# Performance work log

Hardware: AMD Instinct MI355X
Metric: run time of the kernel (lower is better)

The kernel has to match this reference:

```python
import jax, jax.numpy as jnp
import numpy as np
from jax import lax

KH = KW = 3
K = KH * KW
STRIDE = 1
PAD = 1
DIL = 1
GN_GROUPS = 32
EPS = 1e-5


def setup_inputs() -> dict:
    key = jax.random.key(0)
    k0, k1, k2 = jax.random.split(key, 3)
    B, C, H, W = 8, 256, 64, 64
    O = 256
    x = jax.random.normal(k0, (B, C, H, W), jnp.float32)
    # offset-predicting conv (DeformConv2dPack.conv_offset); small weights keep offsets ~O(1)
    w_off = jax.random.normal(k1, (2 * K, C, KH, KW), jnp.float32) * 0.01
    b_off = jnp.zeros((2 * K,), jnp.float32)
    w_dcn = jax.random.normal(k2, (O, C, KH, KW), jnp.float32) * (1.0 / np.sqrt(C * K))
    gamma = jnp.ones((O,), jnp.float32)
    beta = jnp.zeros((O,), jnp.float32)
    return {"x": x, "w_off": w_off, "b_off": b_off, "w_dcn": w_dcn, "gamma": gamma, "beta": beta}


def _deform_conv(x, w_off, b_off, w_dcn):
    B, C, H, W = x.shape
    O = w_dcn.shape[0]
    # offsets via standard conv: [B, 2K, Ho, Wo]; channel layout (k, (dy, dx))
    offset = lax.conv_general_dilated(
        x, w_off, (STRIDE, STRIDE), [(PAD, PAD), (PAD, PAD)],
        rhs_dilation=(DIL, DIL), dimension_numbers=("NCHW", "OIHW", "NCHW"))
    offset = offset + b_off[None, :, None, None]
    Ho, Wo = offset.shape[2], offset.shape[3]
    off = offset.reshape(B, K, 2, Ho, Wo)
    ky = jnp.repeat(jnp.arange(KH), KW)  # [K]
    kx = jnp.tile(jnp.arange(KW), KH)    # [K]
    base_y = (jnp.arange(Ho) * STRIDE - PAD)[None, :, None] + (ky * DIL)[:, None, None]  # [K,Ho,1]
    base_x = (jnp.arange(Wo) * STRIDE - PAD)[None, None, :] + (kx * DIL)[:, None, None]  # [K,1,Wo]
    py = off[:, :, 0] + base_y[None].astype(off.dtype)  # [B,K,Ho,Wo]
    px = off[:, :, 1] + base_x[None].astype(off.dtype)

    def sample_one(xi, py_i, px_i):  # xi [C,H,W]; py/px [K,Ho,Wo]
        y0 = jnp.floor(py_i)
        x0 = jnp.floor(px_i)
        dy = py_i - y0
        dx = px_i - x0
        y0i = y0.astype(jnp.int32)
        x0i = x0.astype(jnp.int32)

        def gather(yi, xj, w):
            valid = (yi >= 0) & (yi < H) & (xj >= 0) & (xj < W)
            yc = jnp.clip(yi, 0, H - 1)
            xc = jnp.clip(xj, 0, W - 1)
            return xi[:, yc, xc] * (w * valid)[None]  # [C,K,Ho,Wo]

        return (gather(y0i, x0i, (1 - dy) * (1 - dx))
                + gather(y0i, x0i + 1, (1 - dy) * dx)
                + gather(y0i + 1, x0i, dy * (1 - dx))
                + gather(y0i + 1, x0i + 1, dy * dx))

    cols = jax.vmap(sample_one)(x, py, px)  # [B,C,K,Ho,Wo]
    y = jnp.einsum("ock,bckp->bop", w_dcn.reshape(O, C, K),
                   cols.reshape(B, C, K, Ho * Wo))
    return y.reshape(B, O, Ho, Wo)


def _group_norm(y, gamma, beta):
    B, O, Ho, Wo = y.shape
    g = y.reshape(B, GN_GROUPS, O // GN_GROUPS, Ho, Wo)
    mean = g.mean(axis=(2, 3, 4), keepdims=True)
    var = g.var(axis=(2, 3, 4), keepdims=True)
    yn = ((g - mean) * lax.rsqrt(var + EPS)).reshape(B, O, Ho, Wo)
    return yn * gamma[None, :, None, None] + beta[None, :, None, None]


def reference(x, w_off, b_off, w_dcn, gamma, beta):
    y = _deform_conv(x, w_off, b_off, w_dcn)
    y = _group_norm(y, gamma, beta)
    return y * jnp.tanh(jax.nn.softplus(y))  # Mish
```

## Files before the change

kernel.cpp:

```cpp
#include <hip/hip_runtime.h>
#include <hip/hip_bf16.h>
#include <math.h>

typedef __bf16 bf16x8 __attribute__((ext_vector_type(8)));
typedef float f32x4 __attribute__((ext_vector_type(4)));
typedef unsigned int u32;
typedef u32 u32x4 __attribute__((ext_vector_type(4)));
typedef u32 u32x2 __attribute__((ext_vector_type(2)));


__device__ inline u32 pack2bf16(float a, float b) {
  u32 ua = __float_as_uint(a);
  u32 ub = __float_as_uint(b);
  ua += 0x7fffu + ((ua >> 16) & 1u);
  ub += 0x7fffu + ((ub >> 16) & 1u);
  return (ua >> 16) | (ub & 0xffff0000u);
}

__global__ void prep(const float* __restrict__ w_dcn, const float* __restrict__ w_off,
                     unsigned short* __restrict__ wT4, unsigned short* __restrict__ wOffT,
                     float* __restrict__ stats) {
  size_t id = (size_t)blockIdx.x * 256 + threadIdx.x;
  if (id < 589824) {
    int o  = (int)(id / 2304);
    int ck = (int)(id % 2304);
    int k = ck >> 8, c = ck & 255;
    float v = w_dcn[(size_t)(o * 256 + c) * 9 + k];
    u32 uv = __float_as_uint(v);
    uv += 0x7fffu + ((uv >> 16) & 1u);
    int tile = ck >> 6, kk = ck & 63;
    int lin = o * 128 + kk * 2;
    int swz = lin ^ ((o & 7) << 4);
    *(unsigned short*)((char*)wT4 + (size_t)tile * 32768 + swz) = (unsigned short)(uv >> 16);
  } else if (id < 663552) {
    int r = (int)(id - 589824);
    int tile = r >> 11;
    int rr = r & 2047;
    int o = rr >> 6, kk = rr & 63;
    int k = tile >> 2, cc = tile & 3;
    int c = (cc << 6) + kk;
    float v = (o < 18) ? w_off[(size_t)(o * 256 + c) * 9 + k] : 0.f;
    u32 uv = __float_as_uint(v);
    uv += 0x7fffu + ((uv >> 16) & 1u);
    int swz = (o * 128 + kk * 2) ^ ((o & 7) << 4);
    *(unsigned short*)((char*)wOffT + (size_t)tile * 4096 + swz) = (unsigned short)(uv >> 16);
  } else if (id < 664064) {
    stats[id - 663552] = 0.f;
  }
}

__global__ __launch_bounds__(256) void transpose_x(const float* __restrict__ x,
                                                   unsigned short* __restrict__ xT) {
  __shared__ float tl[64][65];
  int bx = blockIdx.x;
  int b = bx >> 8;
  int y = (bx >> 2) & 63;
  int cb = (bx & 3) << 6;
  int t = threadIdx.x;
  int xi = t & 63, cr = t >> 6;
  size_t base = (((size_t)(b * 256 + cb) * 64 + y) << 6);
#pragma unroll
  for (int rep = 0; rep < 16; ++rep) {
    int cl = rep * 4 + cr;
    tl[cl][xi] = x[base + (size_t)cl * 4096 + xi];
  }
  __syncthreads();
  int xw = t >> 2, c4 = (t & 3) << 4;
  unsigned short* dst = xT + (((size_t)b * 4096) + y * 64 + xw) * 256 + cb + c4;
  u32 pk[8];
#pragma unroll
  for (int e = 0; e < 8; ++e)
    pk[e] = pack2bf16(tl[c4 + 2 * e][xw], tl[c4 + 2 * e + 1][xw]);
  u32x4 v0 = {pk[0], pk[1], pk[2], pk[3]};
  u32x4 v1 = {pk[4], pk[5], pk[6], pk[7]};
  *(u32x4*)dst = v0;
  *((u32x4*)dst + 1) = v1;
}

__global__ __launch_bounds__(256, 2) void conv_offset_mfma(
    const unsigned short* __restrict__ xT, const unsigned short* __restrict__ wOffT,
    float* __restrict__ offs) {
  __shared__ unsigned short A[2][64][64];
  __shared__ unsigned short Bo[2][2048];
  const int bx = blockIdx.x;
  const int lb = ((bx & 7) << 6) + (bx >> 3);
  const int b = lb >> 6;
  const int y = lb & 63;
  const int t = threadIdx.x;
  const int lane = t & 63, wid = t >> 6;
  const unsigned short* xTb = xT + ((size_t)b << 20);
  const int p = t >> 2;
  const int q16 = (t & 3) << 4;

  f32x4 acc[2];
  {
    f32x4 z = {0.f, 0.f, 0.f, 0.f};
    acc[0] = z; acc[1] = z;
  }

  u32x4 ra = {0u,0u,0u,0u}, rb = {0u,0u,0u,0u};

  auto issue = [&](int tt, int d) {
    int k = tt >> 2, cc = tt & 3;
    int ky = k / 3, kx = k - ky * 3;
    int ys = y - 1 + ky;
    int xs = p - 1 + kx;
    bool ok = ((unsigned)ys < 64u) && ((unsigned)xs < 64u);
    u32x4 z = {0u,0u,0u,0u};
    ra = z; rb = z;
    if (ok) {
      const unsigned short* s0 = xTb + (size_t)(((ys << 6) + xs) << 8) + (cc << 6) + q16;
      ra = *(const u32x4*)s0;
      rb = *(const u32x4*)(s0 + 8);
    }
    __builtin_amdgcn_global_load_lds(
        (const __attribute__((address_space(1))) u32*)((const char*)wOffT + ((size_t)tt << 12) + (wid << 10) + (lane << 4)),
        (__attribute__((address_space(3))) u32*)((char*)&Bo[d][0] + (wid << 10)),
        16, 0, 0);
  };
  auto writeA = [&](int d) {
    char* dst = (char*)&A[d][0][0] + p * 128;
    int b0 = (t & 3) << 5;
    int sw = (p & 7) << 4;
    *(u32x4*)(dst + (b0 ^ sw)) = ra;
    *(u32x4*)(dst + ((b0 + 16) ^ sw)) = rb;
  };

  issue(0, 0);
  writeA(0);
  __syncthreads();

  int cur = 0;
  for (int tt = 0; tt < 36; ++tt) {
    if (tt < 35) issue(tt + 1, cur ^ 1);
#pragma unroll
    for (int s = 0; s < 2; ++s) {
      int row = (wid << 4) + (lane & 15);
      int bir = ((s << 6) + ((lane >> 4) << 4)) ^ ((row & 7) << 4);
      bf16x8 a = *(const bf16x8*)((const char*)&A[cur][0][0] + row * 128 + bir);
#pragma unroll
      for (int j = 0; j < 2; ++j) {
        int o = (j << 4) + (lane & 15);
        int kb = ((s << 6) + ((lane >> 4) << 4)) ^ ((o & 7) << 4);
        bf16x8 bv = *(const bf16x8*)((const char*)&Bo[cur][0] + o * 128 + kb);
        acc[j] = __builtin_amdgcn_mfma_f32_16x16x32_bf16(a, bv, acc[j], 0, 0, 0);
      }
    }
    if (tt < 35) writeA(cur ^ 1);
    __syncthreads();
    cur ^= 1;
  }

#pragma unroll
  for (int j = 0; j < 2; ++j) {
    int o = (j << 4) + (lane & 15);
    if (o < 18) {
#pragma unroll
      for (int r = 0; r < 4; ++r) {
        int pl = (wid << 4) + ((lane >> 4) << 2) + r;
        offs[((size_t)b * 4096 + (y << 6) + pl) * 18 + o] = acc[j][r];
      }
    }
  }
}

union Arena {
  struct {
    unsigned short A[2][128][64];
    unsigned short Bt[2][16384];
  } m;
  unsigned short ytile[256][136];
};

__global__ __launch_bounds__(512, 2) void dcn_main(
    const unsigned short* __restrict__ xT, const float* __restrict__ offs,
    const float* __restrict__ boff, const unsigned short* __restrict__ wT4,
    unsigned short* __restrict__ yb, float* __restrict__ stats) {
  __shared__ Arena ar;
  __shared__ unsigned short poffu[128][9][4];
  __shared__ float pw[128][9][4];

  const int bx = blockIdx.x;
  const int lb = ((bx & 7) << 5) + (bx >> 3);
  const int b = lb >> 5;
  const int pxbase = (lb & 31) << 7;
  const int t = threadIdx.x;
  const int lane = t & 63, wid = t >> 6;
  const int wr = wid >> 2, wc = wid & 3;
  const unsigned short* xTb = xT + ((size_t)b << 20);

  for (int idx = t; idx < 1152; idx += 512) {
    int p = idx / 9, k = idx - p * 9;
    int pxg = pxbase + p;
    int yy = pxg >> 6, xx = pxg & 63;
    const float* op = offs + ((size_t)b * 4096 + pxg) * 18 + k * 2;
    int kyi = k / 3, kxi = k - kyi * 3;
    float py = op[0] + boff[k * 2] + (float)(yy - 1 + kyi);
    float pxf = op[1] + boff[k * 2 + 1] + (float)(xx - 1 + kxi);
    float fy = floorf(py), fx = floorf(pxf);
    float dy = py - fy, dx = pxf - fx;
    int y0 = (int)fy, x0 = (int)fx;
    int y1 = y0 + 1, x1 = x0 + 1;
    float vy0 = ((unsigned)y0 < 64u) ? 1.f : 0.f;
    float vy1 = ((unsigned)y1 < 64u) ? 1.f : 0.f;
    float vx0 = ((unsigned)x0 < 64u) ? 1.f : 0.f;
    float vx1 = ((unsigned)x1 < 64u) ? 1.f : 0.f;
    int y0c = min(max(y0, 0), 63), y1c = min(max(y1, 0), 63);
    int x0c = min(max(x0, 0), 63), x1c = min(max(x1, 0), 63);
    poffu[p][k][0] = (unsigned short)((y0c << 6) + x0c);
    poffu[p][k][1] = (unsigned short)((y0c << 6) + x1c);
    poffu[p][k][2] = (unsigned short)((y1c << 6) + x0c);
    poffu[p][k][3] = (unsigned short)((y1c << 6) + x1c);
    pw[p][k][0] = (1.f - dy) * (1.f - dx) * vy0 * vx0;
    pw[p][k][1] = (1.f - dy) * dx * vy0 * vx1;
    pw[p][k][2] = dy * (1.f - dx) * vy1 * vx0;
    pw[p][k][3] = dy * dx * vy1 * vx1;
  }

  f32x4 acc[4][4];
#pragma unroll
  for (int i = 0; i < 4; ++i)
#pragma unroll
    for (int j = 0; j < 4; ++j) {
      f32x4 z = {0.f, 0.f, 0.f, 0.f};
      acc[i][j] = z;
    }

  const int p_my = t >> 2;
  const int cq = (t & 3) << 4;

  __syncthreads();

  u32x4 r00a, r00b, r01a, r01b, r10a, r10b, r11a, r11b;
  float w00, w01, w10, w11;

  auto issueA = [&](int tt) {
    int k = tt >> 2, cc = tt & 3;
    int cb = (cc << 6) + cq;
    const unsigned short* s00 = xTb + ((int)poffu[p_my][k][0] << 8) + cb;
    const unsigned short* s01 = xTb + ((int)poffu[p_my][k][1] << 8) + cb;
    const unsigned short* s10 = xTb + ((int)poffu[p_my][k][2] << 8) + cb;
    const unsigned short* s11 = xTb + ((int)poffu[p_my][k][3] << 8) + cb;
    w00 = pw[p_my][k][0]; w01 = pw[p_my][k][1];
    w10 = pw[p_my][k][2]; w11 = pw[p_my][k][3];
    r00a = *(const u32x4*)s00; r00b = *(const u32x4*)(s00 + 8);
    r01a = *(const u32x4*)s01; r01b = *(const u32x4*)(s01 + 8);
    r10a = *(const u32x4*)s10; r10b = *(const u32x4*)(s10 + 8);
    r11a = *(const u32x4*)s11; r11b = *(const u32x4*)(s11 + 8);
  };
  auto issueB = [&](int tt, int d) {
    const char* src = (const char*)wT4 + ((size_t)tt << 15);
    char* dstb = (char*)&ar.m.Bt[d][0] + (wid << 12);
#pragma unroll
    for (int i2 = 0; i2 < 4; ++i2) {
      __builtin_amdgcn_global_load_lds(
          (const __attribute__((address_space(1))) u32*)(src + (wid << 12) + (i2 << 10) + (lane << 4)),
          (__attribute__((address_space(3))) u32*)(dstb + (i2 << 10)),
          16, 0, 0);
    }
  };
  auto packA = [&](int d) {
    u32 outp[8];
#pragma unroll
    for (int e = 0; e < 8; ++e) {
      u32 u00 = (e < 4) ? r00a[e] : r00b[e - 4];
      u32 u01 = (e < 4) ? r01a[e] : r01b[e - 4];
      u32 u10 = (e < 4) ? r10a[e] : r10b[e - 4];
      u32 u11 = (e < 4) ? r11a[e] : r11b[e - 4];
      float lo = w00 * __uint_as_float(u00 << 16);
      lo = fmaf(w01, __uint_as_float(u01 << 16), lo);
      lo = fmaf(w10, __uint_as_float(u10 << 16), lo);
      lo = fmaf(w11, __uint_as_float(u11 << 16), lo);
      float hi = w00 * __uint_as_float(u00 & 0xffff0000u);
      hi = fmaf(w01, __uint_as_float(u01 & 0xffff0000u), hi);
      hi = fmaf(w10, __uint_as_float(u10 & 0xffff0000u), hi);
      hi = fmaf(w11, __uint_as_float(u11 & 0xffff0000u), hi);
      u32 r;
      asm("v_cvt_pk_bf16_f32 %0, %1, %2" : "=v"(r) : "v"(lo), "v"(hi));
      outp[e] = r;
    }
    char* dst = (char*)&ar.m.A[d][0][0] + p_my * 128;
    int b0 = (t & 3) << 5;
    int sw = (p_my & 7) << 4;
    u32x4 t0 = {outp[0], outp[1], outp[2], outp[3]};
    u32x4 t1 = {outp[4], outp[5], outp[6], outp[7]};
    *(u32x4*)(dst + (b0 ^ sw)) = t0;
    *(u32x4*)(dst + ((b0 + 16) ^ sw)) = t1;
  };

  issueA(0);
  issueB(0, 0);
  packA(0);
  __syncthreads();

  const int rbase = wr << 6;
  const int obase = wc << 6;
  int cur = 0;
  for (int tt = 0; tt < 36; ++tt) {
    if (tt < 35) { issueA(tt + 1); issueB(tt + 1, cur ^ 1); }
    __builtin_amdgcn_s_setprio(1);
#pragma unroll
    for (int s = 0; s < 2; ++s) {
      bf16x8 a[4], bb[4];
#pragma unroll
      for (int i = 0; i < 4; ++i) {
        int row = rbase + (i << 4) + (lane & 15);
        int bir = ((s << 6) + ((lane >> 4) << 4)) ^ ((row & 7) << 4);
        a[i] = *(const bf16x8*)((const char*)&ar.m.A[cur][0][0] + row * 128 + bir);
      }
#pragma unroll
      for (int j = 0; j < 4; ++j) {
        int o = obase + (j << 4) + (lane & 15);
        int kb = ((s << 6) + ((lane >> 4) << 4)) ^ ((o & 7) << 4);
        bb[j] = *(const bf16x8*)((const char*)&ar.m.Bt[cur][0] + o * 128 + kb);
      }
#pragma unroll
      for (int i = 0; i < 4; ++i)
#pragma unroll
        for (int j = 0; j < 4; ++j)
          acc[i][j] = __builtin_amdgcn_mfma_f32_16x16x32_bf16(a[i], bb[j], acc[i][j], 0, 0, 0);
    }
    __builtin_amdgcn_s_setprio(0);
    if (tt < 35) packA(cur ^ 1);
    __syncthreads();
    cur ^= 1;
  }

#pragma unroll
  for (int j = 0; j < 4; ++j) {
    float s1 = 0.f, s2 = 0.f;
#pragma unroll
    for (int i = 0; i < 4; ++i)
#pragma unroll
      for (int r = 0; r < 4; ++r) {
        float v = acc[i][j][r];
        s1 += v;
        s2 += v * v;
      }
    s1 += __shfl_xor(s1, 1, 64);  s2 += __shfl_xor(s2, 1, 64);
    s1 += __shfl_xor(s1, 2, 64);  s2 += __shfl_xor(s2, 2, 64);
    s1 += __shfl_xor(s1, 4, 64);  s2 += __shfl_xor(s2, 4, 64);
    s1 += __shfl_xor(s1, 16, 64); s2 += __shfl_xor(s2, 16, 64);
    s1 += __shfl_xor(s1, 32, 64); s2 += __shfl_xor(s2, 32, 64);
    if ((lane & 0x37) == 0) {
      int g = (obase + (j << 4) + (lane & 15)) >> 3;
      atomicAdd(&stats[((b << 5) + g) * 2 + 0], s1);
      atomicAdd(&stats[((b << 5) + g) * 2 + 1], s2);
    }
  }

#pragma unroll
  for (int i = 0; i < 4; ++i)
#pragma unroll
    for (int j = 0; j < 4; ++j) {
      int o = obase + (j << 4) + (lane & 15);
      int pxr = rbase + (i << 4) + ((lane >> 4) << 2);
      u32 w0, w1;
      asm("v_cvt_pk_bf16_f32 %0, %1, %2" : "=v"(w0) : "v"(acc[i][j][0]), "v"(acc[i][j][1]));
      asm("v_cvt_pk_bf16_f32 %0, %1, %2" : "=v"(w1) : "v"(acc[i][j][2]), "v"(acc[i][j][3]));
      u32x2 wv = {w0, w1};
      *(u32x2*)((char*)ar.ytile + o * 272 + pxr * 2) = wv;
    }
  __syncthreads();
  {
    int o = t >> 1, half = t & 1;
    const char* srcb = (const char*)ar.ytile + o * 272 + (half << 7);
    unsigned short* dst = yb + (((size_t)(b * 256 + o)) << 12) + pxbase + (half << 6);
#pragma unroll
    for (int q = 0; q < 8; ++q)
      *(u32x4*)((char*)dst + (q << 4)) = *(const u32x4*)(srcb + (q << 4));
  }
}

__global__ __launch_bounds__(256) void gn_mish(const unsigned short* __restrict__ yb,
                                               const float* __restrict__ stats,
                                               const float* __restrict__ gamma,
                                               const float* __restrict__ beta,
                                               float* __restrict__ out) {
  int v = blockIdx.x * 512 + threadIdx.x;
#pragma unroll
  for (int it = 0; it < 2; ++it, v += 256) {
    int o = (v >> 9) & 255;
    int b = v >> 17;
    float s1 = stats[((b << 5) + (o >> 3)) * 2 + 0];
    float s2 = stats[((b << 5) + (o >> 3)) * 2 + 1];
    float mean = s1 * (1.f / 32768.f);
    float var = s2 * (1.f / 32768.f) - mean * mean;
    float rstd = rsqrtf(var + 1e-5f);
    float ga = gamma[o] * rstd, be = beta[o] - mean * gamma[o] * rstd;
    u32x4 u = *(const u32x4*)(yb + ((size_t)v << 3));
    float res[8];
#pragma unroll
    for (int e = 0; e < 4; ++e) {
      float va = __uint_as_float(u[e] << 16);
      float vb = __uint_as_float(u[e] & 0xffff0000u);
      float v0 = fmaf(va, ga, be);
      float v1 = fmaf(vb, ga, be);
      float e0 = expf(fminf(v0, 15.f));
      float e1 = expf(fminf(v1, 15.f));
      float n0 = e0 * (e0 + 2.f);
      float n1 = e1 * (e1 + 2.f);
      float m0 = v0 * (n0 / (n0 + 2.f));
      float m1 = v1 * (n1 / (n1 + 2.f));
      if (v0 > 15.f) m0 = v0;
      if (v1 > 15.f) m1 = v1;
      res[2 * e] = m0;
      res[2 * e + 1] = m1;
    }
    f32x4 o0 = {res[0], res[1], res[2], res[3]};
    f32x4 o1 = {res[4], res[5], res[6], res[7]};
    float* dst = out + ((size_t)v << 3);
    *(f32x4*)dst = o0;
    *((f32x4*)dst + 1) = o1;
  }
}

extern "C" void kernel_launch(void* const* d_in, const int* in_sizes, int n_in,
                              void* d_out, int out_size, void* d_ws, size_t ws_size,
                              hipStream_t stream) {
  const float* x     = (const float*)d_in[0];
  const float* w_off = (const float*)d_in[1];
  const float* b_off = (const float*)d_in[2];
  const float* w_dcn = (const float*)d_in[3];
  const float* gamma = (const float*)d_in[4];
  const float* beta  = (const float*)d_in[5];
  float* out = (float*)d_out;
  char* ws = (char*)d_ws;
  unsigned short* xT   = (unsigned short*)(ws);
  unsigned short* yb   = (unsigned short*)(ws + 16777216);
  float* offs          = (float*)(ws + 33554432);
  unsigned short* wT4  = (unsigned short*)(ws + 35913728);
  unsigned short* wOffT= (unsigned short*)(ws + 37093376);
  float* stats         = (float*)(ws + 37240832);
  prep<<<dim3(2594), dim3(256), 0, stream>>>(w_dcn, w_off, wT4, wOffT, stats);
  transpose_x<<<dim3(2048), dim3(256), 0, stream>>>(x, xT);
  conv_offset_mfma<<<dim3(512), dim3(256), 0, stream>>>(xT, wOffT, offs);
  dcn_main<<<dim3(256), dim3(512), 0, stream>>>(xT, offs, b_off, wT4, yb, stats);
  gn_mish<<<dim3(2048), dim3(256), 0, stream>>>(yb, stats, gamma, beta, out);
}
```

Baseline: 138.7 us.

## Warp-specialize DCN GEMM into producer gather waves and consumer MFMA waves

Splits the 8 waves of each block into 4 producer waves, which gather the bilinear samples, build the A tile and issue the weight loads to LDS, and 4 consumer waves, which run all the MFMAs. Each consumer now covers all 128 pixel rows and a 64-channel output slice, so it holds twice as many accumulators. The goal is to overlap the latency-bound gather with matrix compute across different waves instead of interleaving both inside every wave. The cost is half as many MFMA waves and higher register pressure in consumers, which under launch_bounds(512,2) could cause spills.

```diff
diff --git a/kernel.cpp b/kernel.cpp
--- a/kernel.cpp
+++ b/kernel.cpp
@@ -186,8 +186,13 @@
   const int pxbase = (lb & 31) << 7;
   const int t = threadIdx.x;
   const int lane = t & 63, wid = t >> 6;
-  const int wr = wid >> 2, wc = wid & 3;
+  const bool is_cons = (wid < 4);
+  const int obase = (wid & 3) << 6;
   const unsigned short* xTb = xT + ((size_t)b << 20);
+
+  const int q = ((wid & 3) << 6) + lane;
+  const int p_my = q >> 1;
+  const int half = q & 1;
 
   for (int idx = t; idx < 1152; idx += 512) {
     int p = idx / 9, k = idx - p * 9;
@@ -217,158 +222,148 @@
     pw[p][k][3] = dy * dx * vy1 * vx1;
   }
 
-  f32x4 acc[4][4];
-#pragma unroll
-  for (int i = 0; i < 4; ++i)
+  f32x4 acc[8][4];
+#pragma unroll
+  for (int i = 0; i < 8; ++i)
 #pragma unroll
     for (int j = 0; j < 4; ++j) {
       f32x4 z = {0.f, 0.f, 0.f, 0.f};
       acc[i][j] = z;
     }
 
-  const int p_my = t >> 2;
-  const int cq = (t & 3) << 4;
-
   __syncthreads();
 
-  u32x4 r00a, r00b, r01a, r01b, r10a, r10b, r11a, r11b;
-  float w00, w01, w10, w11;
-
-  auto issueA = [&](int tt) {
-    int k = tt >> 2, cc = tt & 3;
-    int cb = (cc << 6) + cq;
-    const unsigned short* s00 = xTb + ((int)poffu[p_my][k][0] << 8) + cb;
-    const unsigned short* s01 = xTb + ((int)poffu[p_my][k][1] << 8) + cb;
-    const unsigned short* s10 = xTb + ((int)poffu[p_my][k][2] << 8) + cb;
-    const unsigned short* s11 = xTb + ((int)poffu[p_my][k][3] << 8) + cb;
-    w00 = pw[p_my][k][0]; w01 = pw[p_my][k][1];
-    w10 = pw[p_my][k][2]; w11 = pw[p_my][k][3];
-    r00a = *(const u32x4*)s00; r00b = *(const u32x4*)(s00 + 8);
-    r01a = *(const u32x4*)s01; r01b = *(const u32x4*)(s01 + 8);
-    r10a = *(const u32x4*)s10; r10b = *(const u32x4*)(s10 + 8);
-    r11a = *(const u32x4*)s11; r11b = *(const u32x4*)(s11 + 8);
+  auto stage = [&](int nt, int d) {
+    int k = nt >> 2, cc = nt & 3;
+    int cb = (cc << 6) + (half << 5);
+    const unsigned short* s0 = xTb + ((int)poffu[p_my][k][0] << 8) + cb;
+    const unsigned short* s1 = xTb + ((int)poffu[p_my][k][1] << 8) + cb;
+    const unsigned short* s2 = xTb + ((int)poffu[p_my][k][2] << 8) + cb;
+    const unsigned short* s3 = xTb + ((int)poffu[p_my][k][3] << 8) + cb;
+    u32x4 r0[4], r1[4], r2[4], r3[4];
+#pragma unroll
+    for (int v = 0; v < 4; ++v) {
+      r0[v] = *(const u32x4*)(s0 + (v << 3));
+      r1[v] = *(const u32x4*)(s1 + (v << 3));
+      r2[v] = *(const u32x4*)(s2 + (v << 3));
+      r3[v] = *(const u32x4*)(s3 + (v << 3));
+    }
+    {
+      const char* src = (const char*)wT4 + ((size_t)nt << 15) + ((wid & 3) << 13);
+      char* dstb = (char*)&ar.m.Bt[d][0] + ((wid & 3) << 13);
+#pragma unroll
+      for (int i2 = 0; i2 < 8; ++i2) {
+        __builtin_amdgcn_global_load_lds(
+            (const __attribute__((address_space(1))) u32*)(src + (i2 << 10) + (lane << 4)),
+            (__attribute__((address_space(3))) u32*)(dstb + (i2 << 10)),
+            16, 0, 0);
+      }
+    }
+    float w0 = pw[p_my][k][0], w1 = pw[p_my][k][1];
+    float w2 = pw[p_my][k][2], w3 = pw[p_my][k][3];
+    char* dst = (char*)&ar.m.A[d][0][0] + p_my * 128;
+    int sw = (p_my & 7) << 4;
+#pragma unroll
+    for (int v = 0; v < 4; ++v) {
+      u32 o4[4];
+#pragma unroll
+      for (int e = 0; e < 4; ++e) {
+        u32 u0 = r0[v][e], u1 = r1[v][e], u2 = r2[v][e], u3 = r3[v][e];
+        float lo = w0 * __uint_as_float(u0 << 16);
+        lo = fmaf(w1, __uint_as_float(u1 << 16), lo);
+        lo = fmaf(w2, __uint_as_float(u2 << 16), lo);
+        lo = fmaf(w3, __uint_as_float(u3 << 16), lo);
+        float hi = w0 * __uint_as_float(u0 & 0xffff0000u);
+        hi = fmaf(w1, __uint_as_float(u1 & 0xffff0000u), hi);
+        hi = fmaf(w2, __uint_as_float(u2 & 0xffff0000u), hi);
+        hi = fmaf(w3, __uint_as_float(u3 & 0xffff0000u), hi);
+        u32 r;
+        asm("v_cvt_pk_bf16_f32 %0, %1, %2" : "=v"(r) : "v"(lo), "v"(hi));
+        o4[e] = r;
+      }
+      u32x4 ov = {o4[0], o4[1], o4[2], o4[3]};
+      *(u32x4*)(dst + (((half << 6) + (v << 4)) ^ sw)) = ov;
+    }
   };
-  auto issueB = [&](int tt, int d) {
-    const char* src = (const char*)wT4 + ((size_t)tt << 15);
-    char* dstb = (char*)&ar.m.Bt[d][0] + (wid << 12);
-#pragma unroll
-    for (int i2 = 0; i2 < 4; ++i2) {
-      __builtin_amdgcn_global_load_lds(
-          (const __attribute__((address_space(1))) u32*)(src + (wid << 12) + (i2 << 10) + (lane << 4)),
-          (__attribute__((address_space(3))) u32*)(dstb + (i2 << 10)),
-          16, 0, 0);
-    }
-  };
-  auto packA = [&](int d) {
-    u32 outp[8];
-#pragma unroll
-    for (int e = 0; e < 8; ++e) {
-      u32 u00 = (e < 4) ? r00a[e] : r00b[e - 4];
-      u32 u01 = (e < 4) ? r01a[e] : r01b[e - 4];
-      u32 u10 = (e < 4) ? r10a[e] : r10b[e - 4];
-      u32 u11 = (e < 4) ? r11a[e] : r11b[e - 4];
-      float lo = w00 * __uint_as_float(u00 << 16);
-      lo = fmaf(w01, __uint_as_float(u01 << 16), lo);
-      lo = fmaf(w10, __uint_as_float(u10 << 16), lo);
-      lo = fmaf(w11, __uint_as_float(u11 << 16), lo);
-      float hi = w00 * __uint_as_float(u00 & 0xffff0000u);
-      hi = fmaf(w01, __uint_as_float(u01 & 0xffff0000u), hi);
-      hi = fmaf(w10, __uint_as_float(u10 & 0xffff0000u), hi);
-      hi = fmaf(w11, __uint_as_float(u11 & 0xffff0000u), hi);
-      u32 r;
-      asm("v_cvt_pk_bf16_f32 %0, %1, %2" : "=v"(r) : "v"(lo), "v"(hi));
-      outp[e] = r;
-    }
-    char* dst = (char*)&ar.m.A[d][0][0] + p_my * 128;
-    int b0 = (t & 3) << 5;
-    int sw = (p_my & 7) << 4;
-    u32x4 t0 = {outp[0], outp[1], outp[2], outp[3]};
-    u32x4 t1 = {outp[4], outp[5], outp[6], outp[7]};
-    *(u32x4*)(dst + (b0 ^ sw)) = t0;
-    *(u32x4*)(dst + ((b0 + 16) ^ sw)) = t1;
-  };
-
-  issueA(0);
-  issueB(0, 0);
-  packA(0);
+
+  if (!is_cons) stage(0, 0);
   __syncthreads();
 
-  const int rbase = wr << 6;
-  const int obase = wc << 6;
   int cur = 0;
   for (int tt = 0; tt < 36; ++tt) {
-    if (tt < 35) { issueA(tt + 1); issueB(tt + 1, cur ^ 1); }
-    __builtin_amdgcn_s_setprio(1);
-#pragma unroll
-    for (int s = 0; s < 2; ++s) {
-      bf16x8 a[4], bb[4];
-#pragma unroll
-      for (int i = 0; i < 4; ++i) {
-        int row = rbase + (i << 4) + (lane & 15);
-        int bir = ((s << 6) + ((lane >> 4) << 4)) ^ ((row & 7) << 4);
-        a[i] = *(const bf16x8*)((const char*)&ar.m.A[cur][0][0] + row * 128 + bir);
-      }
+    if (is_cons) {
+      const char* Abase = (const char*)&ar.m.A[cur][0][0];
+      const char* Bbase = (const char*)&ar.m.Bt[cur][0];
+      __builtin_amdgcn_s_setprio(1);
+#pragma unroll
+      for (int s = 0; s < 2; ++s) {
+        int kx = (s << 6) + ((lane >> 4) << 4);
+        int swl = (lane & 7) << 4;
+        bf16x8 a[8], bb[4];
+#pragma unroll
+        for (int i = 0; i < 8; ++i)
+          a[i] = *(const bf16x8*)(Abase + ((i << 4) + (lane & 15)) * 128 + (kx ^ swl));
+#pragma unroll
+        for (int j = 0; j < 4; ++j)
+          bb[j] = *(const bf16x8*)(Bbase + (obase + (j << 4) + (lane & 15)) * 128 + (kx ^ swl));
+#pragma unroll
+        for (int i = 0; i < 8; ++i)
+#pragma unroll
+          for (int j = 0; j < 4; ++j)
+            acc[i][j] = __builtin_amdgcn_mfma_f32_16x16x32_bf16(a[i], bb[j], acc[i][j], 0, 0, 0);
+      }
+      __builtin_amdgcn_s_setprio(0);
+    } else {
+      if (tt < 35) stage(tt + 1, cur ^ 1);
+    }
+    __syncthreads();
+    cur ^= 1;
+  }
+
+  if (is_cons) {
+#pragma unroll
+    for (int j = 0; j < 4; ++j) {
+      float s1 = 0.f, s2 = 0.f;
+#pragma unroll
+      for (int i = 0; i < 8; ++i)
+#pragma unroll
+        for (int r = 0; r < 4; ++r) {
+          float v = acc[i][j][r];
+          s1 += v;
+          s2 += v * v;
+        }
+      s1 += __shfl_xor(s1, 1, 64);  s2 += __shfl_xor(s2, 1, 64);
+      s1 += __shfl_xor(s1, 2, 64);  s2 += __shfl_xor(s2, 2, 64);
+      s1 += __shfl_xor(s1, 4, 64);  s2 += __shfl_xor(s2, 4, 64);
+      s1 += __shfl_xor(s1, 16, 64); s2 += __shfl_xor(s2, 16, 64);
+      s1 += __shfl_xor(s1, 32, 64); s2 += __shfl_xor(s2, 32, 64);
+      if ((lane & 0x37) == 0) {
+        int g = (obase + (j << 4) + (lane & 15)) >> 3;
+        atomicAdd(&stats[((b << 5) + g) * 2 + 0], s1);
+        atomicAdd(&stats[((b << 5) + g) * 2 + 1], s2);
+      }
+    }
+#pragma unroll
+    for (int i = 0; i < 8; ++i)
 #pragma unroll
       for (int j = 0; j < 4; ++j) {
         int o = obase + (j << 4) + (lane & 15);
-        int kb = ((s << 6) + ((lane >> 4) << 4)) ^ ((o & 7) << 4);
-        bb[j] = *(const bf16x8*)((const char*)&ar.m.Bt[cur][0] + o * 128 + kb);
-      }
-#pragma unroll
-      for (int i = 0; i < 4; ++i)
-#pragma unroll
-        for (int j = 0; j < 4; ++j)
-          acc[i][j] = __builtin_amdgcn_mfma_f32_16x16x32_bf16(a[i], bb[j], acc[i][j], 0, 0, 0);
-    }
-    __builtin_amdgcn_s_setprio(0);
-    if (tt < 35) packA(cur ^ 1);
-    __syncthreads();
-    cur ^= 1;
-  }
-
-#pragma unroll
-  for (int j = 0; j < 4; ++j) {
-    float s1 = 0.f, s2 = 0.f;
-#pragma unroll
-    for (int i = 0; i < 4; ++i)
-#pragma unroll
-      for (int r = 0; r < 4; ++r) {
-        float v = acc[i][j][r];
-        s1 += v;
-        s2 += v * v;
-      }
-    s1 += __shfl_xor(s1, 1, 64);  s2 += __shfl_xor(s2, 1, 64);
-    s1 += __shfl_xor(s1, 2, 64);  s2 += __shfl_xor(s2, 2, 64);
-    s1 += __shfl_xor(s1, 4, 64);  s2 += __shfl_xor(s2, 4, 64);
-    s1 += __shfl_xor(s1, 16, 64); s2 += __shfl_xor(s2, 16, 64);
-    s1 += __shfl_xor(s1, 32, 64); s2 += __shfl_xor(s2, 32, 64);
-    if ((lane & 0x37) == 0) {
-      int g = (obase + (j << 4) + (lane & 15)) >> 3;
-      atomicAdd(&stats[((b << 5) + g) * 2 + 0], s1);
-      atomicAdd(&stats[((b << 5) + g) * 2 + 1], s2);
-    }
-  }
-
-#pragma unroll
-  for (int i = 0; i < 4; ++i)
-#pragma unroll
-    for (int j = 0; j < 4; ++j) {
-      int o = obase + (j << 4) + (lane & 15);
-      int pxr = rbase + (i << 4) + ((lane >> 4) << 2);
-      u32 w0, w1;
-      asm("v_cvt_pk_bf16_f32 %0, %1, %2" : "=v"(w0) : "v"(acc[i][j][0]), "v"(acc[i][j][1]));
-      asm("v_cvt_pk_bf16_f32 %0, %1, %2" : "=v"(w1) : "v"(acc[i][j][2]), "v"(acc[i][j][3]));
-      u32x2 wv = {w0, w1};
-      *(u32x2*)((char*)ar.ytile + o * 272 + pxr * 2) = wv;
-    }
+        int pxr = (i << 4) + ((lane >> 4) << 2);
+        u32 w0, w1;
+        asm("v_cvt_pk_bf16_f32 %0, %1, %2" : "=v"(w0) : "v"(acc[i][j][0]), "v"(acc[i][j][1]));
+        asm("v_cvt_pk_bf16_f32 %0, %1, %2" : "=v"(w1) : "v"(acc[i][j][2]), "v"(acc[i][j][3]));
+        u32x2 wv = {w0, w1};
+        *(u32x2*)((char*)ar.ytile + o * 272 + pxr * 2) = wv;
+      }
+  }
   __syncthreads();
   {
-    int o = t >> 1, half = t & 1;
-    const char* srcb = (const char*)ar.ytile + o * 272 + (half << 7);
-    unsigned short* dst = yb + (((size_t)(b * 256 + o)) << 12) + pxbase + (half << 6);
-#pragma unroll
-    for (int q = 0; q < 8; ++q)
-      *(u32x4*)((char*)dst + (q << 4)) = *(const u32x4*)(srcb + (q << 4));
+    int o = t >> 1, hf = t & 1;
+    const char* srcb = (const char*)ar.ytile + o * 272 + (hf << 7);
+    unsigned short* dst = yb + (((size_t)(b * 256 + o)) << 12) + pxbase + (hf << 6);
+#pragma unroll
+    for (int qq = 0; qq < 8; ++qq)
+      *(u32x4*)((char*)dst + (qq << 4)) = *(const u32x4*)(srcb + (qq << 4));
   }
 }
 
```

Result: faster. 134.0 us (-3.3%).
